# Kernel optimization log

Measured on AMD Instinct MI355X. Metric: run time of the kernel, lower is better.

Reference implementation:

```python
import jax, jax.numpy as jnp
import numpy as np

NUM_HEADS = 16
B, S, D = 2, 2048, 1024


def setup_inputs() -> dict:
    key = jax.random.key(0)
    ks = jax.random.split(key, 6)
    return {
        "q": jax.random.normal(ks[0], (B, S, D), dtype=jnp.float32),
        "k": jax.random.normal(ks[1], (B, S, D), dtype=jnp.float32),
        "v": jax.random.normal(ks[2], (B, S, D), dtype=jnp.float32),
        "wq": jax.random.normal(ks[3], (D, D), dtype=jnp.float32) * (1.0 / np.sqrt(D)),
        "wk": jax.random.normal(ks[4], (D, D), dtype=jnp.float32) * (1.0 / np.sqrt(D)),
        "wv": jax.random.normal(ks[5], (D, D), dtype=jnp.float32) * (1.0 / np.sqrt(D)),
    }


def reference(q, k, v, wq, wk, wv):
    b, s, d = q.shape
    h = NUM_HEADS
    hd = d // h

    def proj(x, w):
        # torch Linear (no bias): x @ w.T ; chunk(dim=2) == reshape to heads
        return (x @ w.T).reshape(b, s, h, hd).transpose(0, 2, 1, 3)  # [b,h,s,hd]

    qh, kh, vh = proj(q, wq), proj(k, wk), proj(v, wv)
    scale = 1.0 / jnp.sqrt(jnp.asarray(hd, q.dtype))
    scores = jnp.einsum("bhqd,bhkd->bhqk", qh, kh) * scale  # [b,h,s,s]
    # faithful to torch: .tril() zeroes (not -inf) the upper triangle pre-softmax
    mask = jnp.tril(jnp.ones((s, s), dtype=bool))
    scores = jnp.where(mask, scores, jnp.asarray(0.0, scores.dtype))
    attn = jax.nn.softmax(scores, axis=-1)
    out = jnp.einsum("bhqk,bhkd->bhqd", attn, vh)  # [b,h,s,hd]
    return out.transpose(0, 2, 1, 3).reshape(b, s, d)
```

## Files before the change

kernel.cpp:

```cpp
#include <hip/hip_runtime.h>
#include <math.h>

#define B_  2
#define S_  2048
#define D_  1024
#define H_  16
#define HD_ 64
#define NT_ (S_/64)
#define C2_ (0.125f * 1.44269504088896f)

typedef __attribute__((ext_vector_type(8))) _Float16 f16x8;
typedef __attribute__((ext_vector_type(2))) __fp16 h16x2;
typedef __attribute__((ext_vector_type(4))) float f32x4;
typedef unsigned short u16;
typedef unsigned int   u32;

__device__ inline u16 f2h(float f) {
    union { _Float16 h; u16 u; } c; c.h = (_Float16)f;
    return c.u;
}
__device__ inline float h2f(u16 h) {
    union { u16 u; _Float16 h; } c; c.u = h;
    return (float)c.h;
}
__device__ inline u32 pkrtz(float a, float b) {
    union { h16x2 h; u32 u; } c;
    c.h = __builtin_amdgcn_cvt_pkrtz(a, b);
    return c.u;
}

#define GLOAD_LDS16(g, l)                                                    \
    __builtin_amdgcn_global_load_lds(                                        \
        (const __attribute__((address_space(1))) void*)(g),                  \
        (__attribute__((address_space(3))) void*)(l), 16, 0, 0)

__global__ __launch_bounds__(256)
void precast(const float* __restrict__ wq, const float* __restrict__ wk,
             const float* __restrict__ wv, const float* __restrict__ q,
             const float* __restrict__ k,  const float* __restrict__ v,
             u16* __restrict__ Wq, u16* __restrict__ Wk, u16* __restrict__ Wv,
             u16* __restrict__ Xq, u16* __restrict__ Xk, u16* __restrict__ Xv)
{
    const int z = blockIdx.y;
    const size_t n = (z >= 3) ? (size_t)B_ * S_ * D_ : (size_t)D_ * D_;
    const size_t i = ((size_t)blockIdx.x * 256 + threadIdx.x) * 4;
    if (i >= n) return;
    const float* src = (z == 0) ? wq : (z == 1) ? wk : (z == 2) ? wv
                     : (z == 3) ? q  : (z == 4) ? k  : v;
    u16* dst = (z == 0) ? Wq : (z == 1) ? Wk : (z == 2) ? Wv
             : (z == 3) ? Xq : (z == 4) ? Xk : Xv;
    float4 xv = *(const float4*)&src[i];
    *(ushort4*)&dst[i] = make_ushort4(f2h(xv.x), f2h(xv.y), f2h(xv.z), f2h(xv.w));
}

__global__ __launch_bounds__(256)
void proj_all(const u16* __restrict__ Xq, const u16* __restrict__ Xk,
              const u16* __restrict__ Xv, const u16* __restrict__ Wq,
              const u16* __restrict__ Wk, const u16* __restrict__ Wv,
              u16* __restrict__ QP, u16* __restrict__ KP, u16* __restrict__ VT)
{
    const int bid = blockIdx.x;
    const int z   = bid % 3;
    const int rem = bid / 3;
    const int nx  = rem & 7;
    const int ny  = rem >> 3;
    const u16* X = (z == 0) ? Xq : (z == 1) ? Xk : Xv;
    const u16* W = (z == 0) ? Wq : (z == 1) ? Wk : Wv;

    __shared__ u16 Xs[128 * 64];
    __shared__ u16 Ws[128 * 64];

    const int tid  = threadIdx.x;
    const int w    = tid >> 6;
    const int lane = tid & 63;
    const int quad = lane >> 4;
    const int lr   = lane & 15;
    const int m0   = ny * 128;
    const int n0   = nx * 128;

    const int srow  = w * 32 + (lane >> 3);
    const int gslot = (lane & 7) ^ ((lane >> 3) & 7);
    const size_t xbase = (size_t)(m0 + srow) * D_ + gslot * 8;
    const size_t wbase = (size_t)(n0 + srow) * D_ + gslot * 8;
    const int ldsoff = w * 2048 + lane * 8;

    f32x4 acc[2][8];
    #pragma unroll
    for (int i = 0; i < 2; ++i)
        #pragma unroll
        for (int j = 0; j < 8; ++j) acc[i][j] = (f32x4){0.f, 0.f, 0.f, 0.f};

    for (int k0 = 0; k0 < D_; k0 += 64) {
        __syncthreads();
        #pragma unroll
        for (int c = 0; c < 4; ++c) {
            GLOAD_LDS16(X + xbase + (size_t)c * 8 * D_ + k0, &Xs[ldsoff + c * 512]);
            GLOAD_LDS16(W + wbase + (size_t)c * 8 * D_ + k0, &Ws[ldsoff + c * 512]);
        }
        __syncthreads();

        #pragma unroll
        for (int ch = 0; ch < 2; ++ch) {
            const int sl = ((ch * 4 + quad) ^ (lr & 7)) * 8;
            f16x8 a[2];
            #pragma unroll
            for (int i = 0; i < 2; ++i)
                a[i] = *(const f16x8*)&Xs[(w * 32 + i * 16 + lr) * 64 + sl];
            #pragma unroll
            for (int j = 0; j < 8; ++j) {
                f16x8 b = *(const f16x8*)&Ws[(j * 16 + lr) * 64 + sl];
                #pragma unroll
                for (int i = 0; i < 2; ++i)
                    acc[i][j] = __builtin_amdgcn_mfma_f32_16x16x32_f16(a[i], b, acc[i][j], 0, 0, 0);
            }
        }
    }

    if (z < 2) {
        u16* P = (z == 0) ? QP : KP;
        const float sc = (z == 0) ? C2_ : 1.0f;
        #pragma unroll
        for (int i = 0; i < 2; ++i)
            #pragma unroll
            for (int j = 0; j < 8; ++j) {
                int n = n0 + j * 16 + lr;
                int h = n >> 6, hd = n & 63;
                #pragma unroll
                for (int r = 0; r < 4; ++r) {
                    int m = m0 + w * 32 + i * 16 + quad * 4 + r;
                    int b = m >> 11, s = m & (S_ - 1);
                    P[(((size_t)b * H_ + h) * S_ + s) * HD_ + hd] = f2h(acc[i][j][r] * sc);
                }
            }
    } else {
        #pragma unroll
        for (int i = 0; i < 2; ++i)
            #pragma unroll
            for (int j = 0; j < 8; ++j) {
                int n  = n0 + j * 16 + lr;
                int h  = n >> 6, vd = n & 63;
                int m  = m0 + w * 32 + i * 16 + quad * 4;
                int b  = m >> 11, s = m & (S_ - 1);
                ushort4 pv = make_ushort4(f2h(acc[i][j][0]), f2h(acc[i][j][1]),
                                          f2h(acc[i][j][2]), f2h(acc[i][j][3]));
                *(ushort4*)&VT[(((size_t)b * H_ + h) * HD_ + vd) * S_ + s] = pv;
            }
    }
}

__global__ __launch_bounds__(64)
void vtilesum_kernel(const u16* __restrict__ VT, float* __restrict__ TS)
{
    const int t = blockIdx.x, bh = blockIdx.y, vd = threadIdx.x;
    const u16* p = VT + ((size_t)bh * HD_ + vd) * S_ + t * 64;
    float acc = 0.f;
    #pragma unroll
    for (int c = 0; c < 8; ++c) {
        f16x8 vv = *(const f16x8*)&p[c * 8];
        #pragma unroll
        for (int j = 0; j < 8; ++j) acc += (float)vv[j];
    }
    TS[((size_t)bh * NT_ + t) * HD_ + vd] = acc;
}

__global__ __launch_bounds__(64)
void vsuffix_kernel(const float* __restrict__ TS, float* __restrict__ SUF)
{
    const int bh = blockIdx.x, c = threadIdx.x;
    float acc = 0.f;
    SUF[((size_t)bh * (NT_ + 1) + NT_) * HD_ + c] = 0.f;
    for (int t = NT_ - 1; t >= 0; --t) {
        acc += TS[((size_t)bh * NT_ + t) * HD_ + c];
        SUF[((size_t)bh * (NT_ + 1) + t) * HD_ + c] = acc;
    }
}

__global__ __launch_bounds__(256)
void attn_mfma(const u16* __restrict__ QP, const u16* __restrict__ KP,
               const u16* __restrict__ VT, const float* __restrict__ SUF,
               float* __restrict__ OUT)
{
    const int bh = blockIdx.x;
    const int tq = NT_ - 1 - (int)blockIdx.y;
    const int b  = bh >> 4, h = bh & 15;

    __shared__ u16 Ks[64][72];
    __shared__ u16 Vth[64][72];
    __shared__ u16 Phi[4][16][72];

    const int tid  = threadIdx.x;
    const int w    = tid >> 6;
    const int lane = tid & 63;
    const int quad = lane >> 4;
    const int lr   = lane & 15;
    const int r    = tid >> 2;
    const int cb   = (tid & 3) * 16;

    const u16* Qb = QP + (size_t)bh * S_ * HD_;
    const u16* Kb = KP + (size_t)bh * S_ * HD_;
    const u16* Vb = VT + (size_t)bh * HD_ * S_;

    const int q0 = tq * 64;

    f16x8 qf[2];
    #pragma unroll
    for (int ch = 0; ch < 2; ++ch)
        qf[ch] = *(const f16x8*)(Qb + (size_t)(q0 + w * 16 + lr) * HD_ +
                                 ch * 32 + quad * 8);

    f32x4 of[4];
    #pragma unroll
    for (int n = 0; n < 4; ++n) of[n] = (f32x4){0.f, 0.f, 0.f, 0.f};
    float l_i = 0.f;

    f16x8 kpre[2], vpre[2];
    #pragma unroll
    for (int c = 0; c < 2; ++c) {
        kpre[c] = *(const f16x8*)(Kb + (size_t)r * HD_ + cb + c * 8);
        vpre[c] = *(const f16x8*)(Vb + (size_t)r * S_ + cb + c * 8);
    }

    for (int t = 0; t <= tq; ++t) {
        const int k0t = t * 64;
        __syncthreads();
        #pragma unroll
        for (int c = 0; c < 2; ++c) {
            *(f16x8*)&Ks[r][cb + c * 8]  = kpre[c];
            *(f16x8*)&Vth[r][cb + c * 8] = vpre[c];
        }
        __syncthreads();
        if (t < tq) {
            const int kn = k0t + 64;
            #pragma unroll
            for (int c = 0; c < 2; ++c) {
                kpre[c] = *(const f16x8*)(Kb + (size_t)(kn + r) * HD_ + cb + c * 8);
                vpre[c] = *(const f16x8*)(Vb + (size_t)r * S_ + kn + cb + c * 8);
            }
        }

        f32x4 sf[4];
        #pragma unroll
        for (int f = 0; f < 4; ++f) sf[f] = (f32x4){0.f, 0.f, 0.f, 0.f};
        #pragma unroll
        for (int ch = 0; ch < 2; ++ch)
            #pragma unroll
            for (int f = 0; f < 4; ++f) {
                f16x8 ak = *(const f16x8*)&Ks[f * 16 + lr][ch * 32 + quad * 8];
                sf[f] = __builtin_amdgcn_mfma_f32_16x16x32_f16(ak, qf[ch], sf[f], 0, 0, 0);
            }

        if (t == tq) {
            const int ig = q0 + w * 16 + lr;
            #pragma unroll
            for (int f = 0; f < 4; ++f)
                #pragma unroll
                for (int i = 0; i < 4; ++i) {
                    int jg = k0t + f * 16 + quad * 4 + i;
                    sf[f][i] = (jg <= ig) ? sf[f][i] : 0.f;
                }
        }

        float ps = 0.f;
        #pragma unroll
        for (int f = 0; f < 4; ++f)
            #pragma unroll
            for (int i = 0; i < 4; ++i) {
                float p = exp2f(sf[f][i]);
                sf[f][i] = p;
                ps += p;
            }
        ps += __shfl_xor(ps, 16);
        ps += __shfl_xor(ps, 32);
        l_i += ps;

        #pragma unroll
        for (int f = 0; f < 4; ++f) {
            *(u32*)&Phi[w][lr][f * 16 + quad * 4]     = pkrtz(sf[f][0], sf[f][1]);
            *(u32*)&Phi[w][lr][f * 16 + quad * 4 + 2] = pkrtz(sf[f][2], sf[f][3]);
        }

        #pragma unroll
        for (int ch = 0; ch < 2; ++ch) {
            f16x8 pb = *(const f16x8*)&Phi[w][lr][ch * 32 + quad * 8];
            #pragma unroll
            for (int n = 0; n < 4; ++n) {
                f16x8 av = *(const f16x8*)&Vth[n * 16 + lr][ch * 32 + quad * 8];
                of[n] = __builtin_amdgcn_mfma_f32_16x16x32_f16(av, pb, of[n], 0, 0, 0);
            }
        }
    }

    const int cnt = S_ - (q0 + 64);
    const float* suf = SUF + ((size_t)bh * (NT_ + 1) + (tq + 1)) * HD_;
    float inv = 1.0f / (l_i + (float)cnt);
    const int srow = q0 + w * 16 + lr;
    #pragma unroll
    for (int n = 0; n < 4; ++n) {
        float4 sv = *(const float4*)&suf[n * 16 + quad * 4];
        float4 ov;
        ov.x = (of[n][0] + sv.x) * inv;
        ov.y = (of[n][1] + sv.y) * inv;
        ov.z = (of[n][2] + sv.z) * inv;
        ov.w = (of[n][3] + sv.w) * inv;
        *(float4*)&OUT[((size_t)b * S_ + srow) * D_ + h * HD_ + n * 16 + quad * 4] = ov;
    }
}

extern "C" void kernel_launch(void* const* d_in, const int* in_sizes, int n_in,
                              void* d_out, int out_size, void* d_ws, size_t ws_size,
                              hipStream_t stream)
{
    (void)in_sizes; (void)n_in; (void)out_size; (void)ws_size;
    const float* q  = (const float*)d_in[0];
    const float* k  = (const float*)d_in[1];
    const float* v  = (const float*)d_in[2];
    const float* wq = (const float*)d_in[3];
    const float* wk = (const float*)d_in[4];
    const float* wv = (const float*)d_in[5];
    float* out = (float*)d_out;

    const size_t PROJ = (size_t)B_ * H_ * S_ * HD_;
    const size_t WSZ  = (size_t)D_ * D_;
    u16* QP = (u16*)d_ws;
    u16* KP = QP + PROJ;
    u16* VT = KP + PROJ;
    u16* Xq = VT + PROJ;
    u16* Xk = Xq + PROJ;
    u16* Xv = Xk + PROJ;
    u16* Wq = Xv + PROJ;
    u16* Wk = Wq + WSZ;
    u16* Wv = Wk + WSZ;
    float* TS  = (float*)(Wv + WSZ);
    float* SUF = TS + (size_t)B_ * H_ * NT_ * HD_;

    precast<<<dim3(PROJ / 1024, 6), 256, 0, stream>>>(
        wq, wk, wv, q, k, v, Wq, Wk, Wv, Xq, Xk, Xv);
    proj_all<<<dim3(3 * (D_ / 128) * ((B_ * S_) / 128)), 256, 0, stream>>>(
        Xq, Xk, Xv, Wq, Wk, Wv, QP, KP, VT);
    vtilesum_kernel<<<dim3(NT_, B_ * H_), 64, 0, stream>>>(VT, TS);
    vsuffix_kernel<<<B_ * H_, 64, 0, stream>>>(TS, SUF);
    attn_mfma<<<dim3(B_ * H_, NT_), 256, 0, stream>>>(QP, KP, VT, SUF, out);
}
```

Baseline: 199.0 us.

## Fuse activation fp32-to-fp16 cast into projection GEMM with prefetch and block swizzle

The separate precast pass over the q/k/v activations is removed. The projection kernel now loads fp32 activations directly into registers, converts them to fp16 and writes them into swizzled LDS. The weight tile is double-buffered, and the next activation and weight slices are prefetched during the current MFMA loop. Block indices are remapped so that blocks sharing an X row-tile land in different groups. This avoids the write and re-read of the fp16 activation copies, at the cost of more registers and twice as many fp32 global reads per GEMM tile.

```diff
diff --git a/kernel.cpp b/kernel.cpp
--- a/kernel.cpp
+++ b/kernel.cpp
@@ -19,15 +19,19 @@
     union { _Float16 h; u16 u; } c; c.h = (_Float16)f;
     return c.u;
 }
-__device__ inline float h2f(u16 h) {
-    union { u16 u; _Float16 h; } c; c.u = h;
-    return (float)c.h;
-}
 __device__ inline u32 pkrtz(float a, float b) {
     union { h16x2 h; u32 u; } c;
     c.h = __builtin_amdgcn_cvt_pkrtz(a, b);
     return c.u;
 }
+__device__ inline f16x8 cvt8(float4 a, float4 b) {
+    f16x8 r;
+    r[0] = (_Float16)a.x; r[1] = (_Float16)a.y;
+    r[2] = (_Float16)a.z; r[3] = (_Float16)a.w;
+    r[4] = (_Float16)b.x; r[5] = (_Float16)b.y;
+    r[6] = (_Float16)b.z; r[7] = (_Float16)b.w;
+    return r;
+}
 
 #define GLOAD_LDS16(g, l)                                                    \
     __builtin_amdgcn_global_load_lds(                                        \
@@ -35,52 +39,54 @@
         (__attribute__((address_space(3))) void*)(l), 16, 0, 0)
 
 __global__ __launch_bounds__(256)
-void precast(const float* __restrict__ wq, const float* __restrict__ wk,
-             const float* __restrict__ wv, const float* __restrict__ q,
-             const float* __restrict__ k,  const float* __restrict__ v,
-             u16* __restrict__ Wq, u16* __restrict__ Wk, u16* __restrict__ Wv,
-             u16* __restrict__ Xq, u16* __restrict__ Xk, u16* __restrict__ Xv)
+void precastW(const float* __restrict__ wq, const float* __restrict__ wk,
+              const float* __restrict__ wv,
+              u16* __restrict__ Wq, u16* __restrict__ Wk, u16* __restrict__ Wv)
 {
     const int z = blockIdx.y;
-    const size_t n = (z >= 3) ? (size_t)B_ * S_ * D_ : (size_t)D_ * D_;
     const size_t i = ((size_t)blockIdx.x * 256 + threadIdx.x) * 4;
-    if (i >= n) return;
-    const float* src = (z == 0) ? wq : (z == 1) ? wk : (z == 2) ? wv
-                     : (z == 3) ? q  : (z == 4) ? k  : v;
-    u16* dst = (z == 0) ? Wq : (z == 1) ? Wk : (z == 2) ? Wv
-             : (z == 3) ? Xq : (z == 4) ? Xk : Xv;
+    const float* src = (z == 0) ? wq : (z == 1) ? wk : wv;
+    u16* dst = (z == 0) ? Wq : (z == 1) ? Wk : Wv;
     float4 xv = *(const float4*)&src[i];
     *(ushort4*)&dst[i] = make_ushort4(f2h(xv.x), f2h(xv.y), f2h(xv.z), f2h(xv.w));
 }
 
 __global__ __launch_bounds__(256)
-void proj_all(const u16* __restrict__ Xq, const u16* __restrict__ Xk,
-              const u16* __restrict__ Xv, const u16* __restrict__ Wq,
+void proj_all(const float* __restrict__ q, const float* __restrict__ k,
+              const float* __restrict__ v, const u16* __restrict__ Wq,
               const u16* __restrict__ Wk, const u16* __restrict__ Wv,
               u16* __restrict__ QP, u16* __restrict__ KP, u16* __restrict__ VT)
 {
-    const int bid = blockIdx.x;
-    const int z   = bid % 3;
-    const int rem = bid / 3;
+    const int bid = (int)blockIdx.x;
+    const int swz = (bid & 7) * 96 + (bid >> 3);
+    const int z   = swz >> 8;
+    const int rem = swz & 255;
+    const int ny  = rem >> 3;
     const int nx  = rem & 7;
-    const int ny  = rem >> 3;
-    const u16* X = (z == 0) ? Xq : (z == 1) ? Xk : Xv;
-    const u16* W = (z == 0) ? Wq : (z == 1) ? Wk : Wv;
+
+    const float* X = (z == 0) ? q  : (z == 1) ? k  : v;
+    const u16*   W = (z == 0) ? Wq : (z == 1) ? Wk : Wv;
 
     __shared__ u16 Xs[128 * 64];
-    __shared__ u16 Ws[128 * 64];
+    __shared__ u16 Ws[2][128 * 64];
 
     const int tid  = threadIdx.x;
     const int w    = tid >> 6;
     const int lane = tid & 63;
     const int quad = lane >> 4;
     const int lr   = lane & 15;
+    const int rr   = tid >> 1;
+    const int kb   = (tid & 1) * 32;
     const int m0   = ny * 128;
     const int n0   = nx * 128;
 
+    int woff[4];
+    #pragma unroll
+    for (int c = 0; c < 4; ++c)
+        woff[c] = rr * 64 + ((((kb >> 3) + c) ^ (rr & 7)) << 3);
+
     const int srow  = w * 32 + (lane >> 3);
     const int gslot = (lane & 7) ^ ((lane >> 3) & 7);
-    const size_t xbase = (size_t)(m0 + srow) * D_ + gslot * 8;
     const size_t wbase = (size_t)(n0 + srow) * D_ + gslot * 8;
     const int ldsoff = w * 2048 + lane * 8;
 
@@ -90,14 +96,31 @@
         #pragma unroll
         for (int j = 0; j < 8; ++j) acc[i][j] = (f32x4){0.f, 0.f, 0.f, 0.f};
 
+    float4 xa[8];
+    #pragma unroll
+    for (int c = 0; c < 8; ++c)
+        xa[c] = *(const float4*)&X[(size_t)(m0 + rr) * D_ + kb + c * 4];
+    #pragma unroll
+    for (int c = 0; c < 4; ++c)
+        GLOAD_LDS16(W + wbase + (size_t)c * 8 * D_, &Ws[0][ldsoff + c * 512]);
+
+    int cur = 0;
     for (int k0 = 0; k0 < D_; k0 += 64) {
         __syncthreads();
         #pragma unroll
-        for (int c = 0; c < 4; ++c) {
-            GLOAD_LDS16(X + xbase + (size_t)c * 8 * D_ + k0, &Xs[ldsoff + c * 512]);
-            GLOAD_LDS16(W + wbase + (size_t)c * 8 * D_ + k0, &Ws[ldsoff + c * 512]);
-        }
+        for (int c = 0; c < 4; ++c)
+            *(f16x8*)&Xs[woff[c]] = cvt8(xa[2 * c], xa[2 * c + 1]);
         __syncthreads();
+
+        if (k0 + 64 < D_) {
+            #pragma unroll
+            for (int c = 0; c < 4; ++c)
+                GLOAD_LDS16(W + wbase + (size_t)c * 8 * D_ + k0 + 64,
+                            &Ws[cur ^ 1][ldsoff + c * 512]);
+            #pragma unroll
+            for (int c = 0; c < 8; ++c)
+                xa[c] = *(const float4*)&X[(size_t)(m0 + rr) * D_ + k0 + 64 + kb + c * 4];
+        }
 
         #pragma unroll
         for (int ch = 0; ch < 2; ++ch) {
@@ -108,12 +131,13 @@
                 a[i] = *(const f16x8*)&Xs[(w * 32 + i * 16 + lr) * 64 + sl];
             #pragma unroll
             for (int j = 0; j < 8; ++j) {
-                f16x8 b = *(const f16x8*)&Ws[(j * 16 + lr) * 64 + sl];
+                f16x8 b = *(const f16x8*)&Ws[cur][(j * 16 + lr) * 64 + sl];
                 #pragma unroll
                 for (int i = 0; i < 2; ++i)
                     acc[i][j] = __builtin_amdgcn_mfma_f32_16x16x32_f16(a[i], b, acc[i][j], 0, 0, 0);
             }
         }
+        cur ^= 1;
     }
 
     if (z < 2) {
@@ -324,19 +348,15 @@
     u16* QP = (u16*)d_ws;
     u16* KP = QP + PROJ;
     u16* VT = KP + PROJ;
-    u16* Xq = VT + PROJ;
-    u16* Xk = Xq + PROJ;
-    u16* Xv = Xk + PROJ;
-    u16* Wq = Xv + PROJ;
+    u16* Wq = VT + PROJ;
     u16* Wk = Wq + WSZ;
     u16* Wv = Wk + WSZ;
     float* TS  = (float*)(Wv + WSZ);
     float* SUF = TS + (size_t)B_ * H_ * NT_ * HD_;
 
-    precast<<<dim3(PROJ / 1024, 6), 256, 0, stream>>>(
-        wq, wk, wv, q, k, v, Wq, Wk, Wv, Xq, Xk, Xv);
+    precastW<<<dim3(WSZ / 1024, 3), 256, 0, stream>>>(wq, wk, wv, Wq, Wk, Wv);
     proj_all<<<dim3(3 * (D_ / 128) * ((B_ * S_) / 128)), 256, 0, stream>>>(
-        Xq, Xk, Xv, Wq, Wk, Wv, QP, KP, VT);
+        q, k, v, Wq, Wk, Wv, QP, KP, VT);
     vtilesum_kernel<<<dim3(NT_, B_ * H_), 64, 0, stream>>>(VT, TS);
     vsuffix_kernel<<<B_ * H_, 64, 0, stream>>>(TS, SUF);
     attn_mfma<<<dim3(B_ * H_, NT_), 256, 0, stream>>>(QP, KP, VT, SUF, out);
```

New measurement: 225.4 us. 1.13x slower.
